# Kernel tuning notes

Measured on AMD Instinct MI355X. Metric: run time of the kernel, lower is better.

The kernel has to match this reference:

```python
import jax, jax.numpy as jnp
import numpy as np

BL = 512
Q_DIM = K_DIM = V_DIM = 512
R = 2
C = Q_DIM // R  # 256


def setup_inputs() -> dict:
    key = jax.random.key(0)
    ks = jax.random.split(key, 11)
    L = 32768
    x1 = jax.random.normal(ks[0], (1, Q_DIM, L), dtype=jnp.float32)
    x2 = jax.random.normal(ks[1], (1, Q_DIM, L), dtype=jnp.float32)
    mask = jnp.ones((1, 1, L), dtype=jnp.float32)
    s_in = 1.0 / np.sqrt(Q_DIM)
    s_out = 1.0 / np.sqrt(C)
    Wq = jax.random.normal(ks[2], (C, Q_DIM), dtype=jnp.float32) * s_in
    bq = jax.random.normal(ks[3], (C,), dtype=jnp.float32) * 0.01
    Wk = jax.random.normal(ks[4], (C, K_DIM), dtype=jnp.float32) * s_in
    bk = jax.random.normal(ks[5], (C,), dtype=jnp.float32) * 0.01
    Wv = jax.random.normal(ks[6], (C, V_DIM), dtype=jnp.float32) * s_in
    bv = jax.random.normal(ks[7], (C,), dtype=jnp.float32) * 0.01
    Wo = jax.random.normal(ks[8], (V_DIM, C), dtype=jnp.float32) * s_out
    bo = jax.random.normal(ks[9], (V_DIM,), dtype=jnp.float32) * 0.01
    return {"x1": x1, "x2": x2, "mask": mask, "Wq": Wq, "bq": bq,
            "Wk": Wk, "bk": bk, "Wv": Wv, "bv": bv, "Wo": Wo, "bo": bo}


def _sliding_att(x1, mask, Wq, bq, Wk, bk, Wv, bv, Wo, bo):
    bl = BL
    half = bl // 2
    B, _, L = x1.shape  # B == 1 (asserted in original)
    # 1x1 Conv1d projections == per-position matmuls over channels
    q = jnp.einsum('oc,bcl->bol', Wq, x1) + bq[None, :, None]  # (1,C,L)
    k = jnp.einsum('oc,bcl->bol', Wk, x1) + bk[None, :, None]
    v = jnp.einsum('oc,bcl->bol', Wv, x1) + bv[None, :, None]
    c1 = q.shape[1]
    nb = L // bl  # L chosen as multiple of bl; padding branch is a no-op
    pm = mask[:, 0:1, :]  # (1,1,L)
    # query blocks: (nb, C, bl)
    qb = q.reshape(1, c1, nb, bl).transpose(0, 2, 1, 3).reshape(nb, c1, bl)
    # pad K/V/mask with bl//2 zeros each side, gather overlapping windows of width 2*bl
    k_pad = jnp.pad(k, ((0, 0), (0, 0), (half, half)))[0]      # (C, L+bl)
    v_pad = jnp.pad(v, ((0, 0), (0, 0), (half, half)))[0]
    pm_pad = jnp.pad(pm, ((0, 0), (0, 0), (half, half)))[0, 0]  # (L+bl,)
    idx = jnp.arange(nb)[:, None] * bl + jnp.arange(2 * bl)[None, :]  # (nb, 2bl)
    kw = k_pad[:, idx].transpose(1, 0, 2)  # (nb, C, 2bl)
    vw = v_pad[:, idx].transpose(1, 0, 2)  # (nb, C, 2bl)
    pmw = pm_pad[idx][:, None, :]          # (nb, 1, 2bl)
    # banded window mask: query i attends keys j with i <= j < i+bl (in window coords)
    rows = jnp.arange(bl)[:, None]
    cols = jnp.arange(2 * bl)[None, :]
    wmask = ((cols >= rows) & (cols < rows + bl)).astype(x1.dtype)  # (bl, 2bl)
    fmask = wmask[None, :, :] * pmw  # (nb, bl, 2bl)
    scale = 1.0 / np.sqrt(c1)
    energy = jnp.einsum('ncl,ncm->nlm', qb, kw) * scale  # (nb, bl, 2bl)
    attn = jax.nn.softmax(energy + jnp.log(fmask + 1e-6), axis=-1) * fmask
    out = jnp.einsum('ncm,nlm->ncl', vw, attn)  # (nb, C, bl)
    out = jax.nn.relu(out)
    out = jnp.einsum('oc,ncl->nol', Wo, out) + bo[None, :, None]  # (nb, V, bl)
    out = out[None].transpose(0, 2, 1, 3).reshape(1, Wo.shape[0], nb * bl)
    return out[:, :, :L] * pm


def reference(x1, x2, mask, Wq, bq, Wk, bk, Wv, bv, Wo, bo):
    # x2 is accepted by the original forward but unused in self-attention
    return _sliding_att(x1, mask, Wq, bq, Wk, bk, Wv, bv, Wo, bo)
```

## Files before the change

### kernel.cpp

```cpp
#include <hip/hip_runtime.h>
#include <hip/hip_bf16.h>
#include <math.h>

#define L 32768
#define C 256
#define QD 512
#define SCALE (1.0f/16.0f)

typedef __hip_bfloat16 bf16;
typedef short v8s __attribute__((ext_vector_type(8)));
typedef short v4s __attribute__((ext_vector_type(4)));
typedef float v4f __attribute__((ext_vector_type(4)));

__device__ __forceinline__ void ldst16(void* lds, const void* g) {
    __builtin_amdgcn_global_load_lds(
        (const __attribute__((address_space(1))) unsigned int*)g,
        (__attribute__((address_space(3))) unsigned int*)lds, 16, 0, 0);
}
__device__ __forceinline__ short bfbits(float x) {
    bf16 h = __float2bfloat16(x);
    return *reinterpret_cast<short*>(&h);
}

__global__ __launch_bounds__(256) void prep(
    const float* __restrict__ Wq, const float* __restrict__ Wk,
    const float* __restrict__ Wv, const float* __restrict__ bq,
    const float* __restrict__ bk, const float* __restrict__ bv,
    const float* __restrict__ Wo,
    bf16* __restrict__ Wall, bf16* __restrict__ Wob, float* __restrict__ ball)
{
    int i = blockIdx.x * 256 + threadIdx.x;
    if (i < 768*512) {
        int row = i >> 9, idx = i & 511;
        const float* src = row < 256 ? Wq : row < 512 ? Wk : Wv;
        Wall[i] = __float2bfloat16(src[(row & 255) * 512 + idx]);
    } else if (i < 768*512 + 512*256) {
        int j = i - 768*512;
        Wob[j] = __float2bfloat16(Wo[j]);
    } else if (i < 768*512 + 512*256 + 768) {
        int j = i - 768*512 - 512*256;
        ball[j] = j < 256 ? bq[j] : j < 512 ? bk[j - 256] : bv[j - 512];
    }
}

__global__ __launch_bounds__(256) void convt(
    const float* __restrict__ x, short* __restrict__ xT)
{
    __shared__ short st[64*72];
    const int t = threadIdx.x;
    const int l0 = blockIdx.x * 64, c0 = blockIdx.y * 64;
    #pragma unroll
    for (int i = 0; i < 2; i++) {
        int v = i*256 + t;
        int c = v >> 3, l8 = (v & 7) << 3;
        const float* p = x + (size_t)(c0 + c) * L + l0 + l8;
        float4 f0 = *(const float4*)p;
        float4 f1 = *(const float4*)(p + 4);
        bf16* stb = (bf16*)st;
        stb[(l8+0)*72 + c] = __float2bfloat16(f0.x);
        stb[(l8+1)*72 + c] = __float2bfloat16(f0.y);
        stb[(l8+2)*72 + c] = __float2bfloat16(f0.z);
        stb[(l8+3)*72 + c] = __float2bfloat16(f0.w);
        stb[(l8+4)*72 + c] = __float2bfloat16(f1.x);
        stb[(l8+5)*72 + c] = __float2bfloat16(f1.y);
        stb[(l8+6)*72 + c] = __float2bfloat16(f1.z);
        stb[(l8+7)*72 + c] = __float2bfloat16(f1.w);
    }
    __syncthreads();
    #pragma unroll
    for (int i = 0; i < 2; i++) {
        int v = i*256 + t;
        int l = v >> 3, c8 = (v & 7) << 3;
        *(v8s*)(xT + (size_t)(l0 + l) * QD + c0 + c8) = *(const v8s*)&st[l*72 + c8];
    }
}

__global__ __launch_bounds__(256) void qkv_gemm(
    const bf16* __restrict__ A, const bf16* __restrict__ B,
    const float* __restrict__ ball,
    bf16* __restrict__ qT, bf16* __restrict__ kT, bf16* __restrict__ vB)
{
    __shared__ short sA[128*32];
    __shared__ short sB[128*32];
    __shared__ short sE[128*136];

    const int t    = threadIdx.x;
    const int lane = t & 63;
    const int w    = t >> 6;
    const int wm   = w & 1, wn = w >> 1;
    const int col  = lane & 15, quad = lane >> 4;
    const int n0   = blockIdx.x * 128;
    const int my   = blockIdx.y;
    const int m0   = my * 128;

    v4f acc[4][4];
    #pragma unroll
    for (int i = 0; i < 4; i++)
        #pragma unroll
        for (int j = 0; j < 4; j++) acc[i][j] = (v4f){0.f,0.f,0.f,0.f};

    for (int k0 = 0; k0 < QD; k0 += 32) {
        #pragma unroll
        for (int j = 0; j < 2; j++) {
            int idx = j*256 + t;
            int m = idx >> 2, k8 = (idx & 3) << 3;
            ldst16(&sA[idx*8], A + (size_t)(m0 + m) * QD + k0 + k8);
        }
        #pragma unroll
        for (int j = 0; j < 2; j++) {
            int idx = j*256 + t;
            int n = idx >> 2, k8 = (idx & 3) << 3;
            ldst16(&sB[idx*8], B + (size_t)(n0 + n) * QD + k0 + k8);
        }
        __syncthreads();
        v8s af[4], bf[4];
        #pragma unroll
        for (int mt = 0; mt < 4; mt++)
            af[mt] = *(const v8s*)&sA[(wm*64 + mt*16 + col)*32 + quad*8];
        #pragma unroll
        for (int nt = 0; nt < 4; nt++)
            bf[nt] = *(const v8s*)&sB[(wn*64 + nt*16 + col)*32 + quad*8];
        #pragma unroll
        for (int mt = 0; mt < 4; mt++)
            #pragma unroll
            for (int nt = 0; nt < 4; nt++)
                acc[mt][nt] = __builtin_amdgcn_mfma_f32_16x16x32_bf16(af[mt], bf[nt], acc[mt][nt], 0, 0, 0);
        __syncthreads();
    }

    float bias_v[4][4];
    #pragma unroll
    for (int mt = 0; mt < 4; mt++)
        #pragma unroll
        for (int r = 0; r < 4; r++)
            bias_v[mt][r] = ball[m0 + wm*64 + mt*16 + quad*4 + r];

    bf16* sEb = (bf16*)sE;
    if (my < 4) {
        #pragma unroll
        for (int mt = 0; mt < 4; mt++)
            #pragma unroll
            for (int nt = 0; nt < 4; nt++)
                #pragma unroll
                for (int r = 0; r < 4; r++)
                    sEb[(wn*64 + nt*16 + col)*136 + wm*64 + mt*16 + quad*4 + r] =
                        __float2bfloat16(acc[mt][nt][r] + bias_v[mt][r]);
        __syncthreads();
        bf16* dst = (my < 2) ? qT : kT;
        const int c0 = (my & 1) * 128;
        #pragma unroll
        for (int j = 0; j < 8; j++) {
            int idx = j*256 + t;
            int n = idx >> 4, c8 = (idx & 15) << 3;
            *(v8s*)(dst + (size_t)(n0 + n) * C + c0 + c8) = *(const v8s*)&sE[n*136 + c8];
        }
    } else {
        #pragma unroll
        for (int mt = 0; mt < 4; mt++)
            #pragma unroll
            for (int nt = 0; nt < 4; nt++)
                #pragma unroll
                for (int r = 0; r < 4; r++)
                    sEb[(wm*64 + mt*16 + quad*4 + r)*136 + wn*64 + nt*16 + col] =
                        __float2bfloat16(acc[mt][nt][r] + bias_v[mt][r]);
        __syncthreads();
        const int c0 = (my - 4) * 128;
        #pragma unroll
        for (int j = 0; j < 8; j++) {
            int idx = j*256 + t;
            int m = idx >> 4, n8 = (idx & 15) << 3;
            *(v8s*)(vB + (size_t)(c0 + m) * L + n0 + n8) = *(const v8s*)&sE[m*136 + n8];
        }
    }
}

__global__ __launch_bounds__(256) void out_gemm(
    const bf16* __restrict__ A, const bf16* __restrict__ B,
    const float* __restrict__ bo, const float* __restrict__ mask,
    float* __restrict__ out)
{
    __shared__ short sA[128*32];
    __shared__ short sB[128*32];
    __shared__ float sEf[64*132];

    const int t    = threadIdx.x;
    const int lane = t & 63;
    const int w    = t >> 6;
    const int wm   = w & 1, wn = w >> 1;
    const int col  = lane & 15, quad = lane >> 4;
    const int n0   = blockIdx.x * 128;
    const int m0   = blockIdx.y * 128;

    v4f acc[4][4];
    #pragma unroll
    for (int i = 0; i < 4; i++)
        #pragma unroll
        for (int j = 0; j < 4; j++) acc[i][j] = (v4f){0.f,0.f,0.f,0.f};

    for (int k0 = 0; k0 < C; k0 += 32) {
        #pragma unroll
        for (int j = 0; j < 2; j++) {
            int idx = j*256 + t;
            int m = idx >> 2, k8 = (idx & 3) << 3;
            ldst16(&sA[idx*8], A + (size_t)(m0 + m) * C + k0 + k8);
        }
        #pragma unroll
        for (int j = 0; j < 2; j++) {
            int idx = j*256 + t;
            int n = idx >> 2, k8 = (idx & 3) << 3;
            ldst16(&sB[idx*8], B + (size_t)(n0 + n) * C + k0 + k8);
        }
        __syncthreads();
        v8s af[4], bf[4];
        #pragma unroll
        for (int mt = 0; mt < 4; mt++)
            af[mt] = *(const v8s*)&sA[(wm*64 + mt*16 + col)*32 + quad*8];
        #pragma unroll
        for (int nt = 0; nt < 4; nt++)
            bf[nt] = *(const v8s*)&sB[(wn*64 + nt*16 + col)*32 + quad*8];
        #pragma unroll
        for (int mt = 0; mt < 4; mt++)
            #pragma unroll
            for (int nt = 0; nt < 4; nt++)
                acc[mt][nt] = __builtin_amdgcn_mfma_f32_16x16x32_bf16(af[mt], bf[nt], acc[mt][nt], 0, 0, 0);
        __syncthreads();
    }

    #pragma unroll
    for (int half = 0; half < 2; half++) {
        if (wm == half) {
            #pragma unroll
            for (int mt = 0; mt < 4; mt++) {
                #pragma unroll
                for (int r = 0; r < 4; r++) {
                    float bb = bo[m0 + half*64 + mt*16 + quad*4 + r];
                    #pragma unroll
                    for (int nt = 0; nt < 4; nt++)
                        sEf[(mt*16 + quad*4 + r)*132 + wn*64 + nt*16 + col] =
                            acc[mt][nt][r] + bb;
                }
            }
        }
        __syncthreads();
        #pragma unroll
        for (int j = 0; j < 8; j++) {
            int idx = j*256 + t;
            int row = idx >> 5, s4 = (idx & 31) << 2;
            float4 vv = *(const float4*)&sEf[row*132 + s4];
            float4 mk = *(const float4*)&mask[n0 + s4];
            vv.x *= mk.x; vv.y *= mk.y; vv.z *= mk.z; vv.w *= mk.w;
            *(float4*)&out[(size_t)(m0 + half*64 + row) * L + n0 + s4] = vv;
        }
        __syncthreads();
    }
}

__device__ __forceinline__ void load_chunk(
    const short* __restrict__ kT, const short* __restrict__ vB,
    int a0, int t, v8s kreg[4], v8s vreg[4])
{
    #pragma unroll
    for (int j = 0; j < 4; j++) {
        int idx = j*512 + t;
        int r = idx >> 5, s = idx & 31;
        int a = a0 + r;
        v8s kv = {0,0,0,0,0,0,0,0};
        if (a >= 0 && a < L) kv = *(const v8s*)(kT + (size_t)a * C + s*8);
        kreg[j] = kv;
    }
    if (a0 >= 0 && a0 + 63 < L) {
        #pragma unroll
        for (int j = 0; j < 4; j++) {
            int idx = j*512 + t;
            int c = idx >> 3, s = idx & 7;
            vreg[j] = *(const v8s*)(vB + (size_t)c * L + a0 + s*8);
        }
    } else {
        #pragma unroll
        for (int j = 0; j < 4; j++) {
            int idx = j*512 + t;
            int c = idx >> 3, s = idx & 7;
            v8s val;
            #pragma unroll
            for (int e2 = 0; e2 < 8; e2++) {
                int a = a0 + s*8 + e2;
                val[e2] = (a >= 0 && a < L) ? vB[(size_t)c * L + a] : (short)0;
            }
            vreg[j] = val;
        }
    }
}

__device__ __forceinline__ void store_chunk(
    short* __restrict__ sK, short* __restrict__ sVt, int t,
    const v8s kreg[4], const v8s vreg[4])
{
    #pragma unroll
    for (int j = 0; j < 4; j++) {
        int idx = j*512 + t;
        int r = idx >> 5, s = idx & 31;
        *(v8s*)&sK[r*264 + s*8] = kreg[j];
    }
    #pragma unroll
    for (int j = 0; j < 4; j++) {
        int idx = j*512 + t;
        int c = idx >> 3, s = idx & 7;
        *(v8s*)&sVt[c*72 + s*8] = vreg[j];
    }
}

__global__ __launch_bounds__(512, 2) void attn_mfma(
    const bf16* __restrict__ qT, const bf16* __restrict__ kT,
    const bf16* __restrict__ vB, const float* __restrict__ mask,
    bf16* __restrict__ aoT)
{
    __shared__ short sK [64*264];
    __shared__ short sVt[256*72];
    __shared__ short sP [8][16*72];

    const int t    = threadIdx.x;
    const int w    = t >> 6;
    const int lane = t & 63;
    const int col  = lane & 15;
    const int quad = lane >> 4;
    const int bx   = blockIdx.x;
    const int tile = ((bx & 7) << 5) | (bx >> 3);
    const int p0   = tile * 128;
    const int abase = p0 - 256;

    v8s qf[8];
    {
        const short* qp = (const short*)qT + (size_t)(p0 + w*16 + col) * C + quad*8;
        #pragma unroll
        for (int ks = 0; ks < 8; ks++) qf[ks] = *(const v8s*)(qp + ks*32);
    }

    v4f oacc[16];
    #pragma unroll
    for (int i = 0; i < 16; i++) oacc[i] = (v4f){0.f, 0.f, 0.f, 0.f};
    float mrow[4] = {-1e30f, -1e30f, -1e30f, -1e30f};
    float lrow[4] = {0.f, 0.f, 0.f, 0.f};

    v8s kreg[4], vreg[4];
    load_chunk((const short*)kT, (const short*)vB, abase, t, kreg, vreg);
    store_chunk(sK, sVt, t, kreg, vreg);
    __syncthreads();

    for (int ch = 0; ch < 10; ch++) {
        const int a0 = abase + ch*64;
        const bool pf = (ch < 9);
        if (pf)
            load_chunk((const short*)kT, (const short*)vB, a0 + 64, t, kreg, vreg);

        v4f e[4];
        #pragma unroll
        for (int nt = 0; nt < 4; nt++) {
            v4f acc = {0.f, 0.f, 0.f, 0.f};
            const short* kp = &sK[(nt*16 + col)*264 + quad*8];
            #pragma unroll
            for (int ks = 0; ks < 8; ks++) {
                v8s bfrag = *(const v8s*)(kp + ks*32);
                acc = __builtin_amdgcn_mfma_f32_16x16x32_bf16(qf[ks], bfrag, acc, 0, 0, 0);
            }
            e[nt] = acc;
        }

        float cmax[4] = {-1e30f, -1e30f, -1e30f, -1e30f};
        #pragma unroll
        for (int nt = 0; nt < 4; nt++) {
            int a  = a0 + nt*16 + col;
            int aa = ch*64 + nt*16 + col;
            float mval = (a >= 0 && a < L) ? mask[a] : 0.f;
            #pragma unroll
            for (int r = 0; r < 4; r++) {
                int rel = aa - (w*16 + quad*4 + r);
                bool valid = ((unsigned)rel < 512u) && (mval > 0.f);
                float ev = valid ? e[nt][r] * SCALE : -1e30f;
                e[nt][r] = ev;
                cmax[r] = fmaxf(cmax[r], ev);
            }
        }
        #pragma unroll
        for (int off = 1; off < 16; off <<= 1) {
            #pragma unroll
            for (int r = 0; r < 4; r++)
                cmax[r] = fmaxf(cmax[r], __shfl_xor(cmax[r], off));
        }

        float alpha[4];
        #pragma unroll
        for (int r = 0; r < 4; r++) {
            float mnew = fmaxf(mrow[r], cmax[r]);
            alpha[r] = __expf(mrow[r] - mnew);
            mrow[r] = mnew;
        }

        float psum[4] = {0.f, 0.f, 0.f, 0.f};
        bf16* sPw = (bf16*)sP[w];
        #pragma unroll
        for (int nt = 0; nt < 4; nt++) {
            #pragma unroll
            for (int r = 0; r < 4; r++) {
                float ev = e[nt][r];
                float p = (ev > -9e29f) ? __expf(ev - mrow[r]) : 0.f;
                psum[r] += p;
                sPw[(quad*4 + r)*72 + nt*16 + col] = __float2bfloat16(p);
            }
        }
        #pragma unroll
        for (int off = 1; off < 16; off <<= 1) {
            #pragma unroll
            for (int r = 0; r < 4; r++)
                psum[r] += __shfl_xor(psum[r], off);
        }
        #pragma unroll
        for (int r = 0; r < 4; r++) lrow[r] = lrow[r]*alpha[r] + psum[r];

        {
            int src = (col >> 2) << 4;
            float a0b = __shfl(alpha[0], src);
            float a1b = __shfl(alpha[1], src);
            float a2b = __shfl(alpha[2], src);
            float a3b = __shfl(alpha[3], src);
            int rr = col & 3;
            float aO = (rr == 0) ? a0b : (rr == 1) ? a1b : (rr == 2) ? a2b : a3b;
            #pragma unroll
            for (int i = 0; i < 16; i++) {
                oacc[i][0] *= aO; oacc[i][1] *= aO;
                oacc[i][2] *= aO; oacc[i][3] *= aO;
            }
        }

        {
            const short* sPws = (const short*)sP[w];
            v8s pf0 = *(const v8s*)&sPws[col*72 + quad*8];
            v8s pf1 = *(const v8s*)&sPws[col*72 + quad*8 + 32];
            #pragma unroll
            for (int ct = 0; ct < 16; ct++) {
                const short* vp = &sVt[(ct*16 + col)*72 + quad*8];
                v8s vf0 = *(const v8s*)vp;
                v8s vf1 = *(const v8s*)(vp + 32);
                oacc[ct] = __builtin_amdgcn_mfma_f32_16x16x32_bf16(vf0, pf0, oacc[ct], 0, 0, 0);
                oacc[ct] = __builtin_amdgcn_mfma_f32_16x16x32_bf16(vf1, pf1, oacc[ct], 0, 0, 0);
            }
        }

        if (pf) {
            __syncthreads();
            store_chunk(sK, sVt, t, kreg, vreg);
            __syncthreads();
        }
    }

    {
        int src = (col >> 2) << 4;
        float l0b = __shfl(lrow[0], src);
        float l1b = __shfl(lrow[1], src);
        float l2b = __shfl(lrow[2], src);
        float l3b = __shfl(lrow[3], src);
        int rr = col & 3;
        float lO = (rr == 0) ? l0b : (rr == 1) ? l1b : (rr == 2) ? l2b : l3b;
        float inv = (lO > 0.f) ? 1.f / lO : 0.f;
        const int qg = p0 + w*16 + col;
        short* aorow = (short*)aoT + (size_t)qg * C;
        #pragma unroll
        for (int ct = 0; ct < 16; ct++) {
            v4s pk;
            #pragma unroll
            for (int r = 0; r < 4; r++)
                pk[r] = bfbits(fmaxf(oacc[ct][r] * inv, 0.f));
            *(v4s*)(aorow + ct*16 + quad*4) = pk;
        }
    }
}

extern "C" void kernel_launch(void* const* d_in, const int* in_sizes, int n_in,
                              void* d_out, int out_size, void* d_ws, size_t ws_size,
                              hipStream_t stream)
{
    const float* x1   = (const float*)d_in[0];
    const float* mask = (const float*)d_in[2];
    const float* Wq   = (const float*)d_in[3];
    const float* bq   = (const float*)d_in[4];
    const float* Wk   = (const float*)d_in[5];
    const float* bk   = (const float*)d_in[6];
    const float* Wv   = (const float*)d_in[7];
    const float* bv   = (const float*)d_in[8];
    const float* Wo   = (const float*)d_in[9];
    const float* bo   = (const float*)d_in[10];
    float* out = (float*)d_out;

    bf16* x1T  = (bf16*)d_ws;
    bf16* Wall = x1T + (size_t)L * QD;
    bf16* Wob  = Wall + 768*512;
    float* ball = (float*)(Wob + 512*256);
    bf16* qT   = (bf16*)(ball + 768);
    bf16* kT   = qT + (size_t)L * C;
    bf16* vB   = kT + (size_t)L * C;
    bf16* aoT  = vB + (size_t)L * C;

    dim3 blk(256);
    prep<<<dim3((768*512 + 512*256 + 768 + 255)/256), blk, 0, stream>>>(
        Wq, Wk, Wv, bq, bk, bv, Wo, Wall, Wob, ball);
    convt<<<dim3(L/64, QD/64), blk, 0, stream>>>(x1, (short*)x1T);
    qkv_gemm<<<dim3(L/128, 6), blk, 0, stream>>>(Wall, x1T, ball, qT, kT, vB);
    attn_mfma<<<dim3(L/128), dim3(512), 0, stream>>>(qT, kT, vB, mask, aoT);
    out_gemm<<<dim3(L/128, 4), blk, 0, stream>>>(Wob, aoT, bo, mask, out);
}
```

Baseline: 292.0 us.

## Double-buffer K/V LDS tiles and make chunk loads branch-free with clamping

The K and V shared-memory tiles are doubled, so the next chunk is written into the alternate buffer while the current one is consumed. This removes one block-wide barrier per iteration. Boundary handling in the global loads now clamps indices instead of branching or using a scalar per-element fallback. That is safe only because out-of-range keys get zero probability from the mask. The larger LDS footprint forces launch bounds down to one block per CU, which halves occupancy and may reduce latency hiding.

Result: no change. 290.9 us (-0.4%).

```diff
diff --git a/kernel.cpp b/kernel.cpp
--- a/kernel.cpp
+++ b/kernel.cpp
@@ -263,31 +263,15 @@
     for (int j = 0; j < 4; j++) {
         int idx = j*512 + t;
         int r = idx >> 5, s = idx & 31;
-        int a = a0 + r;
-        v8s kv = {0,0,0,0,0,0,0,0};
-        if (a >= 0 && a < L) kv = *(const v8s*)(kT + (size_t)a * C + s*8);
-        kreg[j] = kv;
-    }
-    if (a0 >= 0 && a0 + 63 < L) {
-        #pragma unroll
-        for (int j = 0; j < 4; j++) {
-            int idx = j*512 + t;
-            int c = idx >> 3, s = idx & 7;
-            vreg[j] = *(const v8s*)(vB + (size_t)c * L + a0 + s*8);
-        }
-    } else {
-        #pragma unroll
-        for (int j = 0; j < 4; j++) {
-            int idx = j*512 + t;
-            int c = idx >> 3, s = idx & 7;
-            v8s val;
-            #pragma unroll
-            for (int e2 = 0; e2 < 8; e2++) {
-                int a = a0 + s*8 + e2;
-                val[e2] = (a >= 0 && a < L) ? vB[(size_t)c * L + a] : (short)0;
-            }
-            vreg[j] = val;
-        }
+        int a = min(max(a0 + r, 0), L - 1);
+        kreg[j] = *(const v8s*)(kT + (size_t)a * C + s*8);
+    }
+    #pragma unroll
+    for (int j = 0; j < 4; j++) {
+        int idx = j*512 + t;
+        int c = idx >> 3, s = idx & 7;
+        int ab = min(max(a0 + s*8, 0), L - 8);
+        vreg[j] = *(const v8s*)(vB + (size_t)c * L + ab);
     }
 }
 
@@ -309,13 +293,13 @@
     }
 }
 
-__global__ __launch_bounds__(512, 2) void attn_mfma(
+__global__ __launch_bounds__(512, 1) void attn_mfma(
     const bf16* __restrict__ qT, const bf16* __restrict__ kT,
     const bf16* __restrict__ vB, const float* __restrict__ mask,
     bf16* __restrict__ aoT)
 {
-    __shared__ short sK [64*264];
-    __shared__ short sVt[256*72];
+    __shared__ short sK [2][64*264];
+    __shared__ short sVt[2][256*72];
     __shared__ short sP [8][16*72];
 
     const int t    = threadIdx.x;
@@ -341,22 +325,28 @@
     float mrow[4] = {-1e30f, -1e30f, -1e30f, -1e30f};
     float lrow[4] = {0.f, 0.f, 0.f, 0.f};
 
+    const short* kTs = (const short*)kT;
+    const short* vBs = (const short*)vB;
+    bf16* sPw  = (bf16*)sP[w];
+    const short* sPws = (const short*)sP[w];
+
     v8s kreg[4], vreg[4];
-    load_chunk((const short*)kT, (const short*)vB, abase, t, kreg, vreg);
-    store_chunk(sK, sVt, t, kreg, vreg);
+    load_chunk(kTs, vBs, abase, t, kreg, vreg);
+    store_chunk(sK[0], sVt[0], t, kreg, vreg);
     __syncthreads();
 
     for (int ch = 0; ch < 10; ch++) {
-        const int a0 = abase + ch*64;
+        const int a0  = abase + ch*64;
+        const int cur = ch & 1;
         const bool pf = (ch < 9);
         if (pf)
-            load_chunk((const short*)kT, (const short*)vB, a0 + 64, t, kreg, vreg);
+            load_chunk(kTs, vBs, a0 + 64, t, kreg, vreg);
 
         v4f e[4];
         #pragma unroll
         for (int nt = 0; nt < 4; nt++) {
             v4f acc = {0.f, 0.f, 0.f, 0.f};
-            const short* kp = &sK[(nt*16 + col)*264 + quad*8];
+            const short* kp = &sK[cur][(nt*16 + col)*264 + quad*8];
             #pragma unroll
             for (int ks = 0; ks < 8; ks++) {
                 v8s bfrag = *(const v8s*)(kp + ks*32);
@@ -396,7 +386,6 @@
         }
 
         float psum[4] = {0.f, 0.f, 0.f, 0.f};
-        bf16* sPw = (bf16*)sP[w];
         #pragma unroll
         for (int nt = 0; nt < 4; nt++) {
             #pragma unroll
@@ -432,12 +421,11 @@
         }
 
         {
-            const short* sPws = (const short*)sP[w];
             v8s pf0 = *(const v8s*)&sPws[col*72 + quad*8];
             v8s pf1 = *(const v8s*)&sPws[col*72 + quad*8 + 32];
             #pragma unroll
             for (int ct = 0; ct < 16; ct++) {
-                const short* vp = &sVt[(ct*16 + col)*72 + quad*8];
+                const short* vp = &sVt[cur][(ct*16 + col)*72 + quad*8];
                 v8s vf0 = *(const v8s*)vp;
                 v8s vf1 = *(const v8s*)(vp + 32);
                 oacc[ct] = __builtin_amdgcn_mfma_f32_16x16x32_bf16(vf0, pf0, oacc[ct], 0, 0, 0);
@@ -446,8 +434,7 @@
         }
 
         if (pf) {
-            __syncthreads();
-            store_chunk(sK, sVt, t, kreg, vreg);
+            store_chunk(sK[cur ^ 1], sVt[cur ^ 1], t, kreg, vreg);
             __syncthreads();
         }
     }
```
